# Optimization experiments

Measured on AMD Instinct MI355X. Metric: run time of the kernel, lower is better.

The kernel has to match this reference:

```python
import jax, jax.numpy as jnp
import numpy as np

NUM_USERS = 100000
NUM_ITEMS = 50000
HIDDEN = 64
NUM_LAYERS = 3
NUM_EDGES = 1200000
N = NUM_USERS + NUM_ITEMS


def setup_inputs() -> dict:
    key = jax.random.key(0)
    k_e, k_u, k_i, k_w, k_b = jax.random.split(key, 5)
    edge_index = jax.random.randint(k_e, (2, NUM_EDGES), 0, N, dtype=jnp.int32)
    users_emb = jax.random.normal(k_u, (NUM_USERS, HIDDEN), dtype=jnp.float32) * 0.01
    items_emb = jax.random.normal(k_i, (NUM_ITEMS, HIDDEN), dtype=jnp.float32) * 0.01
    # GCNConv linear weights (glorot-ish) and zero biases, stacked over layers
    scale = 1.0 / np.sqrt(HIDDEN)
    Ws = jax.random.uniform(k_w, (NUM_LAYERS, HIDDEN, HIDDEN), dtype=jnp.float32,
                            minval=-scale, maxval=scale)
    bs = jnp.zeros((NUM_LAYERS, HIDDEN), dtype=jnp.float32)
    return {"edge_index": edge_index, "users_emb": users_emb,
            "items_emb": items_emb, "Ws": Ws, "bs": bs}


def reference(edge_index, users_emb, items_emb, Ws, bs):
    # GraphSAGEModel.forward: concat user/item embeddings, run num_layers GCNConv
    # (PyG defaults: add self-loops, symmetric D^-1/2 A D^-1/2 normalization, bias).
    x = jnp.concatenate([users_emb, items_emb], axis=0)  # [N, H]

    self_loops = jnp.arange(N, dtype=edge_index.dtype)
    src = jnp.concatenate([edge_index[0], self_loops])  # [E+N]
    dst = jnp.concatenate([edge_index[1], self_loops])

    ones = jnp.ones(src.shape[0], dtype=x.dtype)
    deg = jax.ops.segment_sum(ones, dst, num_segments=N)  # in-degree incl self loop
    dinv = jnp.where(deg > 0, jax.lax.rsqrt(deg), 0.0)
    norm = dinv[src] * dinv[dst]  # [E+N], graph-constant across layers

    for l in range(NUM_LAYERS):
        h = x @ Ws[l]                       # linear transform [N, H]
        msg = h[src] * norm[:, None]        # gather + scale
        x = jax.ops.segment_sum(msg, dst, num_segments=N) + bs[l]
    return (x[:NUM_USERS], users_emb, x[NUM_USERS:], items_emb)
```

## Files before the change

kernel.cpp:

```cpp
#include <hip/hip_runtime.h>
#include <hip/hip_fp16.h>
#include <type_traits>

#define NU 100000
#define NI 50000
#define NN 150000
#define HH 64
#define NE 1200000

#define SCAN_CHUNK 1024
#define NBLK ((NN + SCAN_CHUNK - 1) / SCAN_CHUNK)

__global__ void k_concat(const float4* __restrict__ users, const float4* __restrict__ items,
                         const float* __restrict__ dinv,
                         __half2* __restrict__ xs, float4* __restrict__ out) {
    int i = blockIdx.x * blockDim.x + threadIdx.x;
    const int TOT = NN * (HH / 4);
    const int UB  = NU * (HH / 4);
    if (i >= TOT) return;
    float4 v;
    if (i < UB) {
        v = users[i];
        out[UB + i] = v;
    } else {
        int j = i - UB;
        v = items[j];
        out[2 * UB + NI * (HH / 4) + j] = v;
    }
    float dv = dinv[i >> 4];
    xs[2 * i]     = __halves2half2(__float2half_rn(v.x * dv), __float2half_rn(v.y * dv));
    xs[2 * i + 1] = __halves2half2(__float2half_rn(v.z * dv), __float2half_rn(v.w * dv));
}

__global__ void k_rank(const int4* __restrict__ dst4, int* __restrict__ counts,
                       int4* __restrict__ rank4) {
    int t = blockIdx.x * blockDim.x + threadIdx.x;
    if (t >= NE / 4) return;
    int4 d = dst4[t];
    int4 r;
    r.x = atomicAdd(&counts[d.x], 1);
    r.y = atomicAdd(&counts[d.y], 1);
    r.z = atomicAdd(&counts[d.z], 1);
    r.w = atomicAdd(&counts[d.w], 1);
    rank4[t] = r;
}

__global__ void k_scan_reduce(const int* __restrict__ counts, int* __restrict__ bsum,
                              float* __restrict__ dinv) {
    __shared__ int sd[256];
    int t = threadIdx.x;
    int base = blockIdx.x * SCAN_CHUNK + t * 4;
    int s = 0;
    if (base + 3 < NN) {
        int4 v = *(const int4*)(counts + base);
        s = v.x + v.y + v.z + v.w;
        dinv[base + 0] = rsqrtf((float)(v.x + 1));
        dinv[base + 1] = rsqrtf((float)(v.y + 1));
        dinv[base + 2] = rsqrtf((float)(v.z + 1));
        dinv[base + 3] = rsqrtf((float)(v.w + 1));
    } else {
        for (int i = 0; i < 4; ++i)
            if (base + i < NN) {
                int c = counts[base + i];
                s += c;
                dinv[base + i] = rsqrtf((float)(c + 1));
            }
    }
    sd[t] = s; __syncthreads();
    for (int off = 128; off > 0; off >>= 1) {
        if (t < off) sd[t] += sd[t + off];
        __syncthreads();
    }
    if (t == 0) bsum[blockIdx.x] = sd[0];
}

__global__ void k_scan_top(int* __restrict__ bsum, int* __restrict__ row_ptr) {
    __shared__ int sd[256];
    int t = threadIdx.x;
    int v = (t < NBLK) ? bsum[t] : 0;
    sd[t] = v; __syncthreads();
    for (int off = 1; off < 256; off <<= 1) {
        int x = (t >= off) ? sd[t - off] : 0;
        __syncthreads();
        sd[t] += x;
        __syncthreads();
    }
    if (t < NBLK) bsum[t] = sd[t] - v;
    if (t == 0) row_ptr[NN] = NE;
}

__global__ void k_scan_chunks(const int* __restrict__ counts, const int* __restrict__ boff,
                              int* __restrict__ row_ptr) {
    __shared__ int sd[256];
    int t = threadIdx.x;
    int base = blockIdx.x * SCAN_CHUNK + t * 4;
    int c[4];
#pragma unroll
    for (int i = 0; i < 4; ++i) c[i] = (base + i < NN) ? counts[base + i] : 0;
    int tt = c[0] + c[1] + c[2] + c[3];
    sd[t] = tt; __syncthreads();
    for (int off = 1; off < 256; off <<= 1) {
        int x = (t >= off) ? sd[t - off] : 0;
        __syncthreads();
        sd[t] += x;
        __syncthreads();
    }
    int off0 = boff[blockIdx.x] + (sd[t] - tt);
    int run = 0;
#pragma unroll
    for (int i = 0; i < 4; ++i) {
        if (base + i < NN) row_ptr[base + i] = off0 + run;
        run += c[i];
    }
}

__global__ void k_fill(const int4* __restrict__ src4, const int4* __restrict__ dst4,
                       const int4* __restrict__ rank4, const int* __restrict__ row_ptr,
                       int* __restrict__ col) {
    int t = blockIdx.x * blockDim.x + threadIdx.x;
    if (t >= NE / 8) return;
    int4 s0 = src4[2 * t],  s1 = src4[2 * t + 1];
    int4 d0 = dst4[2 * t],  d1 = dst4[2 * t + 1];
    int4 r0 = rank4[2 * t], r1 = rank4[2 * t + 1];
    int p0 = row_ptr[d0.x], p1 = row_ptr[d0.y], p2 = row_ptr[d0.z], p3 = row_ptr[d0.w];
    int p4 = row_ptr[d1.x], p5 = row_ptr[d1.y], p6 = row_ptr[d1.z], p7 = row_ptr[d1.w];
    col[p0 + r0.x] = s0.x;
    col[p1 + r0.y] = s0.y;
    col[p2 + r0.z] = s0.z;
    col[p3 + r0.w] = s0.w;
    col[p4 + r1.x] = s1.x;
    col[p5 + r1.y] = s1.y;
    col[p6 + r1.z] = s1.z;
    col[p7 + r1.w] = s1.w;
}

__global__ __launch_bounds__(256) void k_aggregate(const __half* __restrict__ x,
                                                   __half* __restrict__ y,
                                                   const float* __restrict__ dinv,
                                                   const int* __restrict__ row_ptr,
                                                   const int* __restrict__ col) {
    int lane = threadIdx.x & 63;
    int wave = blockIdx.x * 4 + (threadIdx.x >> 6);
    int na = wave * 2;
    if (na >= NN) return;
    int nb = na + 1;
    int q  = lane >> 4;
    int f4 = (lane & 15) << 2;

    float a0 = 0.f, a1 = 0.f, a2 = 0.f, a3 = 0.f;
    float b0 = 0.f, b1 = 0.f, b2 = 0.f, b3 = 0.f;

#define GATHER(r, c0, c1, c2, c3)                                          \
    {                                                                      \
        uint2 raw = *(const uint2*)(x + (size_t)(r) * HH + f4);            \
        float2 f0 = __half22float2(*(__half2*)&raw.x);                     \
        float2 f1 = __half22float2(*(__half2*)&raw.y);                     \
        c0 += f0.x; c1 += f0.y; c2 += f1.x; c3 += f1.y;                    \
    }

    int ea = row_ptr[na], enda = row_ptr[na + 1];
    int eb = enda,        endb = row_ptr[nb + 1];

    {
        int ia = ea + q - 1;
        int ib = eb + q - 1;
        int rA = (q == 0) ? na : ((ia < enda) ? col[ia] : NN);
        int rB = (q == 0) ? nb : ((ib < endb) ? col[ib] : NN);
        GATHER(rA, a0, a1, a2, a3);
        GATHER(rB, b0, b1, b2, b3);
        ea += 3; eb += 3;
    }
    while (ea < enda || eb < endb) {
        int iA1 = ea + q,     iA2 = ea + 4 + q;
        int iB1 = eb + q,     iB2 = eb + 4 + q;
        int rA1 = (iA1 < enda) ? col[iA1] : NN;
        int rA2 = (iA2 < enda) ? col[iA2] : NN;
        int rB1 = (iB1 < endb) ? col[iB1] : NN;
        int rB2 = (iB2 < endb) ? col[iB2] : NN;
        GATHER(rA1, a0, a1, a2, a3);
        GATHER(rA2, a0, a1, a2, a3);
        GATHER(rB1, b0, b1, b2, b3);
        GATHER(rB2, b0, b1, b2, b3);
        ea += 8; eb += 8;
    }
#undef GATHER

    a0 += __shfl_xor(a0, 16); a1 += __shfl_xor(a1, 16);
    a2 += __shfl_xor(a2, 16); a3 += __shfl_xor(a3, 16);
    b0 += __shfl_xor(b0, 16); b1 += __shfl_xor(b1, 16);
    b2 += __shfl_xor(b2, 16); b3 += __shfl_xor(b3, 16);
    a0 += __shfl_xor(a0, 32); a1 += __shfl_xor(a1, 32);
    a2 += __shfl_xor(a2, 32); a3 += __shfl_xor(a3, 32);
    b0 += __shfl_xor(b0, 32); b1 += __shfl_xor(b1, 32);
    b2 += __shfl_xor(b2, 32); b3 += __shfl_xor(b3, 32);

    if (lane < 32) {
        int   n  = (q == 0) ? na : nb;
        float dv = dinv[n];
        float s0 = (q == 0) ? a0 : b0;
        float s1 = (q == 0) ? a1 : b1;
        float s2 = (q == 0) ? a2 : b2;
        float s3 = (q == 0) ? a3 : b3;
        __half2 h0 = __halves2half2(__float2half_rn(dv * s0), __float2half_rn(dv * s1));
        __half2 h1 = __halves2half2(__float2half_rn(dv * s2), __float2half_rn(dv * s3));
        uint2 packed;
        packed.x = *(unsigned int*)&h0;
        packed.y = *(unsigned int*)&h1;
        *(uint2*)(y + (size_t)n * HH + f4) = packed;
    }
}

#define GR 128
#define XSS 65
template <typename OutT>
__global__ __launch_bounds__(256) void k_gemm(const __half* __restrict__ y,
                                              const float* __restrict__ W,
                                              const float* __restrict__ b,
                                              const float* __restrict__ dinv,
                                              OutT* __restrict__ out_lo,
                                              OutT* __restrict__ out_hi,
                                              int split) {
    __shared__ float xs[GR * XSS];
    __shared__ float ws[HH * HH];
    int t = threadIdx.x;
    int rowBase = blockIdx.x * GR;

    {
        const float4* W4 = (const float4*)W;
        float4* ws4 = (float4*)ws;
#pragma unroll
        for (int i = 0; i < 4; ++i) ws4[i * 256 + t] = W4[i * 256 + t];
    }
#pragma unroll
    for (int it = 0; it < 4; ++it) {
        int g = it * 256 + t;
        int r = g >> 3;
        int c0 = (g & 7) * 8;
        int row = rowBase + r;
        if (row < NN) {
            int4 raw = *(const int4*)(y + (size_t)row * HH + c0);
            __half2 h0 = *(__half2*)&raw.x, h1 = *(__half2*)&raw.y;
            __half2 h2 = *(__half2*)&raw.z, h3 = *(__half2*)&raw.w;
            float2 f0 = __half22float2(h0), f1 = __half22float2(h1);
            float2 f2 = __half22float2(h2), f3 = __half22float2(h3);
            float* dp = xs + r * XSS + c0;
            dp[0] = f0.x; dp[1] = f0.y; dp[2] = f1.x; dp[3] = f1.y;
            dp[4] = f2.x; dp[5] = f2.y; dp[6] = f3.x; dp[7] = f3.y;
        }
    }
    __syncthreads();

    int tx = t & 7;
    int ty = t >> 3;
    int j0 = tx * 8;
    int r0 = ty * 4;

    float acc[4][8];
#pragma unroll
    for (int i = 0; i < 4; ++i)
#pragma unroll
        for (int j = 0; j < 8; ++j) acc[i][j] = 0.f;

    for (int k = 0; k < HH; ++k) {
        float4 w0 = *(const float4*)(ws + k * HH + j0);
        float4 w1 = *(const float4*)(ws + k * HH + j0 + 4);
        float wv[8] = {w0.x, w0.y, w0.z, w0.w, w1.x, w1.y, w1.z, w1.w};
#pragma unroll
        for (int i = 0; i < 4; ++i) {
            float xv = xs[(r0 + i) * XSS + k];
#pragma unroll
            for (int j = 0; j < 8; ++j) acc[i][j] += xv * wv[j];
        }
    }

    float bj[8];
#pragma unroll
    for (int j = 0; j < 8; ++j) bj[j] = b[j0 + j];

#pragma unroll
    for (int i = 0; i < 4; ++i) {
        int r = rowBase + r0 + i;
        if (r >= NN) continue;
        if constexpr (std::is_same_v<OutT, float>) {
            float4 o0 = make_float4(acc[i][0] + bj[0], acc[i][1] + bj[1],
                                    acc[i][2] + bj[2], acc[i][3] + bj[3]);
            float4 o1 = make_float4(acc[i][4] + bj[4], acc[i][5] + bj[5],
                                    acc[i][6] + bj[6], acc[i][7] + bj[7]);
            float* d = (r < split) ? ((float*)out_lo + (size_t)r * HH)
                                   : ((float*)out_hi + (size_t)(r - split) * HH);
            *(float4*)(d + j0) = o0;
            *(float4*)(d + j0 + 4) = o1;
        } else {
            float dv = dinv[r];
            __half2 h[4];
#pragma unroll
            for (int j = 0; j < 4; ++j)
                h[j] = __halves2half2(
                    __float2half_rn((acc[i][2 * j]     + bj[2 * j])     * dv),
                    __float2half_rn((acc[i][2 * j + 1] + bj[2 * j + 1]) * dv));
            __half* d = (__half*)out_lo + (size_t)r * HH + j0;
            *(int4*)d = *(int4*)h;
        }
    }
}

extern "C" void kernel_launch(void* const* d_in, const int* in_sizes, int n_in,
                              void* d_out, int out_size, void* d_ws, size_t ws_size,
                              hipStream_t stream) {
    const int*   edge  = (const int*)d_in[0];
    const int*   src   = edge;
    const int*   dst   = edge + NE;
    const float* users = (const float*)d_in[1];
    const float* items = (const float*)d_in[2];
    const float* Ws    = (const float*)d_in[3];
    const float* bs    = (const float*)d_in[4];
    float*       out   = (float*)d_out;

    char* w = (char*)d_ws;
    __half* Xs0     = (__half*)w; w += (size_t)(NN + 1) * HH * 2;
    __half* Xs1     = (__half*)w; w += (size_t)(NN + 1) * HH * 2;
    float*  dinv    = (float*)w;  w += (size_t)NN * 4;
    int*    counts  = (int*)w;    w += (size_t)NN * 4;
    int*    row_ptr = (int*)w;    w += (size_t)(NN + 1) * 4;
    w += 4;
    int*    bsum    = (int*)w;    w += 256 * 4;
    int*    col     = (int*)w;    w += (size_t)NE * 4;
    int*    rank    = (int*)w;    w += (size_t)NE * 4;
    (void)ws_size; (void)in_sizes; (void)n_in; (void)out_size;

    hipMemsetAsync(counts, 0, (size_t)NN * sizeof(int), stream);
    hipMemsetAsync(Xs0 + (size_t)NN * HH, 0, HH * sizeof(__half), stream);
    hipMemsetAsync(Xs1 + (size_t)NN * HH, 0, HH * sizeof(__half), stream);

    k_rank<<<(NE / 4 + 255) / 256, 256, 0, stream>>>((const int4*)dst, counts, (int4*)rank);
    k_scan_reduce<<<NBLK, 256, 0, stream>>>(counts, bsum, dinv);
    k_concat<<<(NN * (HH / 4) + 255) / 256, 256, 0, stream>>>(
        (const float4*)users, (const float4*)items, dinv, (__half2*)Xs0, (float4*)out);
    k_scan_top<<<1, 256, 0, stream>>>(bsum, row_ptr);
    k_scan_chunks<<<NBLK, 256, 0, stream>>>(counts, bsum, row_ptr);
    k_fill<<<(NE / 8 + 255) / 256, 256, 0, stream>>>(
        (const int4*)src, (const int4*)dst, (const int4*)rank, row_ptr, col);

    const int AGG_BLOCKS  = NN / 8;
    const int GEMM_BLOCKS = (NN + GR - 1) / GR;

    k_aggregate<<<AGG_BLOCKS, 256, 0, stream>>>(Xs0, Xs1, dinv, row_ptr, col);
    k_gemm<__half><<<GEMM_BLOCKS, 256, 0, stream>>>(
        Xs1, Ws + 0 * HH * HH, bs + 0 * HH, dinv, Xs0, Xs0, NN);
    k_aggregate<<<AGG_BLOCKS, 256, 0, stream>>>(Xs0, Xs1, dinv, row_ptr, col);
    k_gemm<__half><<<GEMM_BLOCKS, 256, 0, stream>>>(
        Xs1, Ws + 1 * HH * HH, bs + 1 * HH, dinv, Xs0, Xs0, NN);
    k_aggregate<<<AGG_BLOCKS, 256, 0, stream>>>(Xs0, Xs1, dinv, row_ptr, col);
    k_gemm<float><<<GEMM_BLOCKS, 256, 0, stream>>>(
        Xs1, Ws + 2 * HH * HH, bs + 2 * HH, dinv,
        out , out + (size_t)2 * NU * HH , NU);
}
```

Before: 416.7 us.

## Fuse graph preprocessing kernels and use single-pass lookback scan

Replaces the three-kernel row-pointer scan with one kernel that chains block prefixes through a decoupled lookback on a state array. The concat and CSR fill kernels are merged into one launch that splits work by block index. The three memsets become one, since the state and counts buffers are now adjacent, and the Xs0 padding row is zeroed inside k_rank. The goal is to cut launch and inter-kernel gaps in preprocessing, at the cost of spin-waiting between scan blocks, which depends on earlier blocks making forward progress.

Result: slower. 433.0 us (+3.9%).

```diff
diff --git a/kernel.cpp b/kernel.cpp
--- a/kernel.cpp
+++ b/kernel.cpp
@@ -11,92 +11,49 @@
 #define SCAN_CHUNK 1024
 #define NBLK ((NN + SCAN_CHUNK - 1) / SCAN_CHUNK)
 
-__global__ void k_concat(const float4* __restrict__ users, const float4* __restrict__ items,
-                         const float* __restrict__ dinv,
-                         __half2* __restrict__ xs, float4* __restrict__ out) {
-    int i = blockIdx.x * blockDim.x + threadIdx.x;
-    const int TOT = NN * (HH / 4);
-    const int UB  = NU * (HH / 4);
-    if (i >= TOT) return;
-    float4 v;
-    if (i < UB) {
-        v = users[i];
-        out[UB + i] = v;
-    } else {
-        int j = i - UB;
-        v = items[j];
-        out[2 * UB + NI * (HH / 4) + j] = v;
-    }
-    float dv = dinv[i >> 4];
-    xs[2 * i]     = __halves2half2(__float2half_rn(v.x * dv), __float2half_rn(v.y * dv));
-    xs[2 * i + 1] = __halves2half2(__float2half_rn(v.z * dv), __float2half_rn(v.w * dv));
-}
-
-__global__ void k_rank(const int4* __restrict__ dst4, int* __restrict__ counts,
-                       int4* __restrict__ rank4) {
+__global__ __launch_bounds__(256) void k_rank(const int4* __restrict__ dst4,
+                                              int* __restrict__ counts,
+                                              int4* __restrict__ rank4,
+                                              __half* __restrict__ xs_pad) {
+    if (blockIdx.x == 0 && threadIdx.x < 8)
+        ((int4*)xs_pad)[threadIdx.x] = make_int4(0, 0, 0, 0);
     int t = blockIdx.x * blockDim.x + threadIdx.x;
-    if (t >= NE / 4) return;
-    int4 d = dst4[t];
-    int4 r;
-    r.x = atomicAdd(&counts[d.x], 1);
-    r.y = atomicAdd(&counts[d.y], 1);
-    r.z = atomicAdd(&counts[d.z], 1);
-    r.w = atomicAdd(&counts[d.w], 1);
-    rank4[t] = r;
-}
-
-__global__ void k_scan_reduce(const int* __restrict__ counts, int* __restrict__ bsum,
-                              float* __restrict__ dinv) {
+    if (t >= NE / 8) return;
+    int4 d0 = dst4[2 * t], d1 = dst4[2 * t + 1];
+    int4 r0, r1;
+    r0.x = atomicAdd(&counts[d0.x], 1);
+    r0.y = atomicAdd(&counts[d0.y], 1);
+    r0.z = atomicAdd(&counts[d0.z], 1);
+    r0.w = atomicAdd(&counts[d0.w], 1);
+    r1.x = atomicAdd(&counts[d1.x], 1);
+    r1.y = atomicAdd(&counts[d1.y], 1);
+    r1.z = atomicAdd(&counts[d1.z], 1);
+    r1.w = atomicAdd(&counts[d1.w], 1);
+    rank4[2 * t]     = r0;
+    rank4[2 * t + 1] = r1;
+}
+
+__global__ __launch_bounds__(256) void k_scan(const int* __restrict__ counts,
+                                              float* __restrict__ dinv,
+                                              int* __restrict__ row_ptr,
+                                              unsigned int* __restrict__ state) {
     __shared__ int sd[256];
+    __shared__ int s_prefix;
     int t = threadIdx.x;
-    int base = blockIdx.x * SCAN_CHUNK + t * 4;
-    int s = 0;
+    int b = blockIdx.x;
+    int base = b * SCAN_CHUNK + t * 4;
+    int c[4];
     if (base + 3 < NN) {
         int4 v = *(const int4*)(counts + base);
-        s = v.x + v.y + v.z + v.w;
-        dinv[base + 0] = rsqrtf((float)(v.x + 1));
-        dinv[base + 1] = rsqrtf((float)(v.y + 1));
-        dinv[base + 2] = rsqrtf((float)(v.z + 1));
-        dinv[base + 3] = rsqrtf((float)(v.w + 1));
+        c[0] = v.x; c[1] = v.y; c[2] = v.z; c[3] = v.w;
     } else {
-        for (int i = 0; i < 4; ++i)
-            if (base + i < NN) {
-                int c = counts[base + i];
-                s += c;
-                dinv[base + i] = rsqrtf((float)(c + 1));
-            }
-    }
-    sd[t] = s; __syncthreads();
-    for (int off = 128; off > 0; off >>= 1) {
-        if (t < off) sd[t] += sd[t + off];
-        __syncthreads();
-    }
-    if (t == 0) bsum[blockIdx.x] = sd[0];
-}
-
-__global__ void k_scan_top(int* __restrict__ bsum, int* __restrict__ row_ptr) {
-    __shared__ int sd[256];
-    int t = threadIdx.x;
-    int v = (t < NBLK) ? bsum[t] : 0;
-    sd[t] = v; __syncthreads();
-    for (int off = 1; off < 256; off <<= 1) {
-        int x = (t >= off) ? sd[t - off] : 0;
-        __syncthreads();
-        sd[t] += x;
-        __syncthreads();
-    }
-    if (t < NBLK) bsum[t] = sd[t] - v;
-    if (t == 0) row_ptr[NN] = NE;
-}
-
-__global__ void k_scan_chunks(const int* __restrict__ counts, const int* __restrict__ boff,
-                              int* __restrict__ row_ptr) {
-    __shared__ int sd[256];
-    int t = threadIdx.x;
-    int base = blockIdx.x * SCAN_CHUNK + t * 4;
-    int c[4];
-#pragma unroll
-    for (int i = 0; i < 4; ++i) c[i] = (base + i < NN) ? counts[base + i] : 0;
+#pragma unroll
+        for (int i = 0; i < 4; ++i) c[i] = (base + i < NN) ? counts[base + i] : 0;
+    }
+#pragma unroll
+    for (int i = 0; i < 4; ++i)
+        if (base + i < NN) dinv[base + i] = rsqrtf((float)(c[i] + 1));
+
     int tt = c[0] + c[1] + c[2] + c[3];
     sd[t] = tt; __syncthreads();
     for (int off = 1; off < 256; off <<= 1) {
@@ -105,33 +62,85 @@
         sd[t] += x;
         __syncthreads();
     }
-    int off0 = boff[blockIdx.x] + (sd[t] - tt);
+
+    if (t == 0) {
+        unsigned int agg = (unsigned int)sd[255];
+        if (b == 0) {
+            __hip_atomic_store(&state[0], (2u << 30) | agg, __ATOMIC_RELEASE,
+                               __HIP_MEMORY_SCOPE_AGENT);
+            s_prefix = 0;
+        } else {
+            __hip_atomic_store(&state[b], (1u << 30) | agg, __ATOMIC_RELEASE,
+                               __HIP_MEMORY_SCOPE_AGENT);
+            unsigned int prefix = 0;
+            int p = b - 1;
+            while (true) {
+                unsigned int s = __hip_atomic_load(&state[p], __ATOMIC_ACQUIRE,
+                                                   __HIP_MEMORY_SCOPE_AGENT);
+                unsigned int fl = s >> 30;
+                if (fl == 0u) continue;
+                prefix += s & 0x3FFFFFFFu;
+                if (fl == 2u) break;
+                --p;
+            }
+            __hip_atomic_store(&state[b], (2u << 30) | (prefix + agg),
+                               __ATOMIC_RELEASE, __HIP_MEMORY_SCOPE_AGENT);
+            s_prefix = (int)prefix;
+        }
+    }
+    __syncthreads();
+
+    int off0 = s_prefix + (sd[t] - tt);
     int run = 0;
 #pragma unroll
     for (int i = 0; i < 4; ++i) {
         if (base + i < NN) row_ptr[base + i] = off0 + run;
         run += c[i];
     }
-}
-
-__global__ void k_fill(const int4* __restrict__ src4, const int4* __restrict__ dst4,
-                       const int4* __restrict__ rank4, const int* __restrict__ row_ptr,
-                       int* __restrict__ col) {
-    int t = blockIdx.x * blockDim.x + threadIdx.x;
-    if (t >= NE / 8) return;
-    int4 s0 = src4[2 * t],  s1 = src4[2 * t + 1];
-    int4 d0 = dst4[2 * t],  d1 = dst4[2 * t + 1];
-    int4 r0 = rank4[2 * t], r1 = rank4[2 * t + 1];
-    int p0 = row_ptr[d0.x], p1 = row_ptr[d0.y], p2 = row_ptr[d0.z], p3 = row_ptr[d0.w];
-    int p4 = row_ptr[d1.x], p5 = row_ptr[d1.y], p6 = row_ptr[d1.z], p7 = row_ptr[d1.w];
-    col[p0 + r0.x] = s0.x;
-    col[p1 + r0.y] = s0.y;
-    col[p2 + r0.z] = s0.z;
-    col[p3 + r0.w] = s0.w;
-    col[p4 + r1.x] = s1.x;
-    col[p5 + r1.y] = s1.y;
-    col[p6 + r1.z] = s1.z;
-    col[p7 + r1.w] = s1.w;
+    if (b == NBLK - 1 && t == 0) row_ptr[NN] = NE;
+}
+
+#define CONCAT_BLOCKS (NN * (HH / 4) / 256)
+#define FILL_BLOCKS   ((NE / 8 + 255) / 256)
+
+__global__ __launch_bounds__(256) void k_concat_fill(
+    const float4* __restrict__ users, const float4* __restrict__ items,
+    const float* __restrict__ dinv, __half2* __restrict__ xs, float4* __restrict__ out,
+    const int4* __restrict__ src4, const int4* __restrict__ dst4,
+    const int4* __restrict__ rank4, const int* __restrict__ row_ptr,
+    int* __restrict__ col) {
+    if (blockIdx.x < CONCAT_BLOCKS) {
+        int i = blockIdx.x * 256 + threadIdx.x;
+        const int UB = NU * (HH / 4);
+        float4 v;
+        if (i < UB) {
+            v = users[i];
+            out[UB + i] = v;
+        } else {
+            int j = i - UB;
+            v = items[j];
+            out[2 * UB + NI * (HH / 4) + j] = v;
+        }
+        float dv = dinv[i >> 4];
+        xs[2 * i]     = __halves2half2(__float2half_rn(v.x * dv), __float2half_rn(v.y * dv));
+        xs[2 * i + 1] = __halves2half2(__float2half_rn(v.z * dv), __float2half_rn(v.w * dv));
+    } else {
+        int t = (blockIdx.x - CONCAT_BLOCKS) * 256 + threadIdx.x;
+        if (t >= NE / 8) return;
+        int4 s0 = src4[2 * t],  s1 = src4[2 * t + 1];
+        int4 d0 = dst4[2 * t],  d1 = dst4[2 * t + 1];
+        int4 r0 = rank4[2 * t], r1 = rank4[2 * t + 1];
+        int p0 = row_ptr[d0.x], p1 = row_ptr[d0.y], p2 = row_ptr[d0.z], p3 = row_ptr[d0.w];
+        int p4 = row_ptr[d1.x], p5 = row_ptr[d1.y], p6 = row_ptr[d1.z], p7 = row_ptr[d1.w];
+        col[p0 + r0.x] = s0.x;
+        col[p1 + r0.y] = s0.y;
+        col[p2 + r0.z] = s0.z;
+        col[p3 + r0.w] = s0.w;
+        col[p4 + r1.x] = s1.x;
+        col[p5 + r1.y] = s1.y;
+        col[p6 + r1.z] = s1.z;
+        col[p7 + r1.w] = s1.w;
+    }
 }
 
 __global__ __launch_bounds__(256) void k_aggregate(const __half* __restrict__ x,
@@ -320,25 +329,21 @@
     __half* Xs0     = (__half*)w; w += (size_t)(NN + 1) * HH * 2;
     __half* Xs1     = (__half*)w; w += (size_t)(NN + 1) * HH * 2;
     float*  dinv    = (float*)w;  w += (size_t)NN * 4;
+    unsigned int* state = (unsigned int*)w; w += 256 * 4;
     int*    counts  = (int*)w;    w += (size_t)NN * 4;
     int*    row_ptr = (int*)w;    w += (size_t)(NN + 1) * 4;
-    w += 4;
-    int*    bsum    = (int*)w;    w += 256 * 4;
+    w += 12;
     int*    col     = (int*)w;    w += (size_t)NE * 4;
     int*    rank    = (int*)w;    w += (size_t)NE * 4;
     (void)ws_size; (void)in_sizes; (void)n_in; (void)out_size;
 
-    hipMemsetAsync(counts, 0, (size_t)NN * sizeof(int), stream);
-    hipMemsetAsync(Xs0 + (size_t)NN * HH, 0, HH * sizeof(__half), stream);
-    hipMemsetAsync(Xs1 + (size_t)NN * HH, 0, HH * sizeof(__half), stream);
-
-    k_rank<<<(NE / 4 + 255) / 256, 256, 0, stream>>>((const int4*)dst, counts, (int4*)rank);
-    k_scan_reduce<<<NBLK, 256, 0, stream>>>(counts, bsum, dinv);
-    k_concat<<<(NN * (HH / 4) + 255) / 256, 256, 0, stream>>>(
-        (const float4*)users, (const float4*)items, dinv, (__half2*)Xs0, (float4*)out);
-    k_scan_top<<<1, 256, 0, stream>>>(bsum, row_ptr);
-    k_scan_chunks<<<NBLK, 256, 0, stream>>>(counts, bsum, row_ptr);
-    k_fill<<<(NE / 8 + 255) / 256, 256, 0, stream>>>(
+    hipMemsetAsync(state, 0, (size_t)(256 + NN) * sizeof(int), stream);
+
+    k_rank<<<(NE / 8 + 255) / 256, 256, 0, stream>>>(
+        (const int4*)dst, counts, (int4*)rank, Xs0 + (size_t)NN * HH);
+    k_scan<<<NBLK, 256, 0, stream>>>(counts, dinv, row_ptr, state);
+    k_concat_fill<<<CONCAT_BLOCKS + FILL_BLOCKS, 256, 0, stream>>>(
+        (const float4*)users, (const float4*)items, dinv, (__half2*)Xs0, (float4*)out,
         (const int4*)src, (const int4*)dst, (const int4*)rank, row_ptr, col);
 
     const int AGG_BLOCKS  = NN / 8;
```
